# Optimization experiments

Hardware: AMD Instinct MI355X
Metric: run time of the kernel (lower is better)

Reference implementation:

```python
import jax, jax.numpy as jnp
import numpy as np

B, H, W, CIN, COUT, KH, KW = 8, 256, 256, 64, 64, 3, 3

def setup_inputs() -> dict:
    key = jax.random.key(0)
    k1, k2 = jax.random.split(key)
    inputs = jax.random.normal(k1, (B, H, W, CIN), dtype=jnp.float32)
    kernel = jax.random.normal(k2, (CIN, COUT, KH, KW), dtype=jnp.float32)
    return {"inputs": inputs, "kernel": kernel}

def reference(inputs, kernel):
    # Stride-1 transposed convolution with 'full' output size:
    # out[b, p, q, co] = sum_{ci,i,j} inputs[b, i, j, ci] * kernel[ci, co, p-i, q-j]
    # which is a full (mathematical) convolution. lax performs cross-correlation,
    # so flip the kernel spatially and pad by (k-1) on each side.
    kh, kw = kernel.shape[2], kernel.shape[3]
    k_flipped = jnp.flip(kernel, axis=(2, 3))
    out = jax.lax.conv_general_dilated(
        inputs, k_flipped,
        window_strides=(1, 1),
        padding=[(kh - 1, kh - 1), (kw - 1, kw - 1)],
        dimension_numbers=("NHWC", "IOHW", "NHWC"))
    # out: [B, H+KH-1, W+KW-1, COUT]; original call() adds no bias.
    return out
```

## Files before the change

kernel.cpp:

```cpp
#include <hip/hip_runtime.h>
#include <hip/hip_bf16.h>


#define OH 258
#define OW 258

typedef __bf16 bf16x8 __attribute__((ext_vector_type(8)));
typedef float  f32x4  __attribute__((ext_vector_type(4)));

__global__ void prep_w_kernel(const float* __restrict__ k, __bf16* __restrict__ wsW) {
    int i = blockIdx.x * 256 + threadIdx.x;
    int c  = i & 31;
    int co = (i >> 5) & 63;
    int st = i >> 11;
    int s   = st & 1;
    int tap = st >> 1;
    int kh = tap / 3, kw = tap % 3;
    float v = k[(s * 32 + c) * 576 + co * 9 + kh * 3 + kw];
    wsW[i] = (__bf16)v;
}

__global__ __launch_bounds__(1024, 4)
void tconv_kernel(const float* __restrict__ in, const __bf16* __restrict__ wsW,
                  float* __restrict__ out) {
    __shared__ __bf16 lds_in[612 * 64];
    __shared__ __bf16 lds_w[36864];

    const int tid = threadIdx.x;
    const int b  = blockIdx.z;
    const int p0 = blockIdx.y * 32;
    const int q0 = blockIdx.x * 16;

    #pragma unroll 1
    for (int k = 0; k < 5; ++k) {
        const int it = tid + k * 1024;
        const bool act = (k < 4) || (tid < 800);
        int pix = it >> 3, c8 = it & 7;
        int r = pix / 18, c = pix - r * 18;
        int ip = p0 - 2 + r, iq = q0 - 2 + c;
        f32x4 v0 = {0.f,0.f,0.f,0.f}, v1 = {0.f,0.f,0.f,0.f};
        if (act && (unsigned)ip < 256u && (unsigned)iq < 256u) {
            const float* g = in + (((size_t)b * 256 + ip) * 256 + iq) * 64 + c8 * 8;
            v0 = *(const f32x4*)g;
            v1 = *(const f32x4*)(g + 4);
        }
        if (act) {
            bf16x8 w;
            w[0]=(__bf16)v0[0]; w[1]=(__bf16)v0[1]; w[2]=(__bf16)v0[2]; w[3]=(__bf16)v0[3];
            w[4]=(__bf16)v1[0]; w[5]=(__bf16)v1[1]; w[6]=(__bf16)v1[2]; w[7]=(__bf16)v1[3];
            *(bf16x8*)&lds_in[pix * 64 + (c8 ^ (pix & 7)) * 8] = w;
        }
    }
    #pragma unroll
    for (int k = 0; k < 5; ++k) {
        const int g = tid + k * 1024;
        if ((k < 4) || (tid < 512))
            *(bf16x8*)&lds_w[(size_t)g * 8] = *(const bf16x8*)&wsW[(size_t)g * 8];
    }
    __syncthreads();

    const int wv = tid >> 6, lane = tid & 63;
    const int ml = lane & 15, h = lane >> 4;
    const int woff = ml * 32 + h * 8;
    const int rbase = wv * 2;

    f32x4 acc[2][4] = {};

    #pragma unroll 1
    for (int tap = 0; tap < 9; ++tap) {
        const int kh = tap / 3, kw = tap - kh * 3;
        const __bf16* wt = lds_w + tap * 4096;
        #pragma unroll
        for (int s = 0; s < 2; ++s) {
            bf16x8 bfr[4];
            #pragma unroll
            for (int nt = 0; nt < 4; ++nt)
                bfr[nt] = *(const bf16x8*)(wt + s * 2048 + nt * 512 + woff);
            const int j = s * 4 + h;
            #pragma unroll
            for (int mt = 0; mt < 2; ++mt) {
                int row = rbase + mt + 2 - kh;
                int pix = row * 18 + (2 - kw) + ml;
                bf16x8 afr = *(const bf16x8*)&lds_in[pix * 64 + ((j ^ (pix & 7)) * 8)];
                #pragma unroll
                for (int nt = 0; nt < 4; ++nt)
                    acc[mt][nt] = __builtin_amdgcn_mfma_f32_16x16x32_bf16(
                        bfr[nt], afr, acc[mt][nt], 0, 0, 0);
            }
        }
    }

    const int q = q0 + ml;
    #pragma unroll
    for (int mt = 0; mt < 2; ++mt) {
        int p = p0 + rbase + mt;
        if (p < OH && q < OW) {
            float* op = out + (((size_t)b * OH + p) * OW + q) * 64 + h * 4;
            #pragma unroll
            for (int nt = 0; nt < 4; ++nt)
                *(f32x4*)(op + nt * 16) = acc[mt][nt];
        }
    }
}

extern "C" void kernel_launch(void* const* d_in, const int* in_sizes, int n_in,
                              void* d_out, int out_size, void* d_ws, size_t ws_size,
                              hipStream_t stream) {
    (void)in_sizes; (void)n_in; (void)out_size; (void)ws_size;
    const float* in   = (const float*)d_in[0];
    const float* kern = (const float*)d_in[1];
    float* out = (float*)d_out;
    __bf16* wsW = (__bf16*)d_ws;

    prep_w_kernel<<<144, 256, 0, stream>>>(kern, wsW);
    dim3 grid(17, 9, 8);
    tconv_kernel<<<grid, 1024, 0, stream>>>(in, wsW, out);
}
```

Baseline: 257.3 us.

## Make conv kernel persistent with register-prefetched next-tile input patches

Replaces the 1224-block grid with 256 persistent blocks that each loop over 4-5 output tiles. Weights are loaded into LDS once per block, and the next tile's input patch is fetched into registers while the current tile's MFMAs run. The weight prep layout is also reordered so each lane's B-fragment reads are contiguous. The cost is higher register pressure from 40 prefetched float4 values per thread, an extra barrier per tile, and tail imbalance between 5-tile and 4-tile blocks.

```diff
diff --git a/kernel.cpp b/kernel.cpp
--- a/kernel.cpp
+++ b/kernel.cpp
@@ -10,14 +10,44 @@
 
 __global__ void prep_w_kernel(const float* __restrict__ k, __bf16* __restrict__ wsW) {
     int i = blockIdx.x * 256 + threadIdx.x;
-    int c  = i & 31;
-    int co = (i >> 5) & 63;
+    int j  = i & 7;
+    int ml = (i >> 3) & 15;
+    int h  = (i >> 7) & 3;
+    int nt = (i >> 9) & 3;
     int st = i >> 11;
-    int s   = st & 1;
-    int tap = st >> 1;
-    int kh = tap / 3, kw = tap % 3;
-    float v = k[(s * 32 + c) * 576 + co * 9 + kh * 3 + kw];
-    wsW[i] = (__bf16)v;
+    int s  = st & 1, tap = st >> 1;
+    int ci = s * 32 + h * 8 + j;
+    int co = nt * 16 + ml;
+    wsW[i] = (__bf16)k[ci * 576 + co * 9 + tap];
+}
+
+__device__ __forceinline__ void tile_coords(int tau, int& b, int& p0, int& q0) {
+    int bb = tau / 153;
+    int rr = tau - bb * 153;
+    int py = rr / 17;
+    b  = bb;
+    p0 = py * 32;
+    q0 = (rr - py * 17) * 16;
+}
+
+__device__ __forceinline__ void issue_patch_loads(
+        const float* __restrict__ in, int b, int p0, int q0, int tid,
+        f32x4 (&v0)[5], f32x4 (&v1)[5]) {
+    #pragma unroll
+    for (int k = 0; k < 5; ++k) {
+        const int it = tid + k * 1024;
+        const bool act = (k < 4) || (tid < 800);
+        int pix = it >> 3, c8 = it & 7;
+        int r = pix / 18, c = pix - r * 18;
+        int ip = p0 - 2 + r, iq = q0 - 2 + c;
+        f32x4 z = {0.f, 0.f, 0.f, 0.f};
+        v0[k] = z; v1[k] = z;
+        if (act && (unsigned)ip < 256u && (unsigned)iq < 256u) {
+            const float* g = in + (((size_t)b * 256 + ip) * 256 + iq) * 64 + c8 * 8;
+            v0[k] = *(const f32x4*)g;
+            v1[k] = *(const f32x4*)(g + 4);
+        }
+    }
 }
 
 __global__ __launch_bounds__(1024, 4)
@@ -27,79 +57,88 @@
     __shared__ __bf16 lds_w[36864];
 
     const int tid = threadIdx.x;
-    const int b  = blockIdx.z;
-    const int p0 = blockIdx.y * 32;
-    const int q0 = blockIdx.x * 16;
 
-    #pragma unroll 1
-    for (int k = 0; k < 5; ++k) {
-        const int it = tid + k * 1024;
-        const bool act = (k < 4) || (tid < 800);
-        int pix = it >> 3, c8 = it & 7;
-        int r = pix / 18, c = pix - r * 18;
-        int ip = p0 - 2 + r, iq = q0 - 2 + c;
-        f32x4 v0 = {0.f,0.f,0.f,0.f}, v1 = {0.f,0.f,0.f,0.f};
-        if (act && (unsigned)ip < 256u && (unsigned)iq < 256u) {
-            const float* g = in + (((size_t)b * 256 + ip) * 256 + iq) * 64 + c8 * 8;
-            v0 = *(const f32x4*)g;
-            v1 = *(const f32x4*)(g + 4);
-        }
-        if (act) {
-            bf16x8 w;
-            w[0]=(__bf16)v0[0]; w[1]=(__bf16)v0[1]; w[2]=(__bf16)v0[2]; w[3]=(__bf16)v0[3];
-            w[4]=(__bf16)v1[0]; w[5]=(__bf16)v1[1]; w[6]=(__bf16)v1[2]; w[7]=(__bf16)v1[3];
-            *(bf16x8*)&lds_in[pix * 64 + (c8 ^ (pix & 7)) * 8] = w;
-        }
-    }
     #pragma unroll
     for (int k = 0; k < 5; ++k) {
         const int g = tid + k * 1024;
         if ((k < 4) || (tid < 512))
             *(bf16x8*)&lds_w[(size_t)g * 8] = *(const bf16x8*)&wsW[(size_t)g * 8];
     }
-    __syncthreads();
 
     const int wv = tid >> 6, lane = tid & 63;
     const int ml = lane & 15, h = lane >> 4;
-    const int woff = ml * 32 + h * 8;
+    const int woff = h * 128 + ml * 8;
     const int rbase = wv * 2;
 
-    f32x4 acc[2][4] = {};
+    const int bx = blockIdx.x;
+    const int n_t = (bx < 200) ? 5 : 4;
+
+    int cb, cp0, cq0;
+    tile_coords(bx, cb, cp0, cq0);
+    f32x4 v0[5], v1[5];
+    issue_patch_loads(in, cb, cp0, cq0, tid, v0, v1);
+
+    int nb = 0, np0 = 0, nq0 = 0;
 
     #pragma unroll 1
-    for (int tap = 0; tap < 9; ++tap) {
-        const int kh = tap / 3, kw = tap - kh * 3;
-        const __bf16* wt = lds_w + tap * 4096;
+    for (int t = 0; t < n_t; ++t) {
+        __syncthreads();
         #pragma unroll
-        for (int s = 0; s < 2; ++s) {
-            bf16x8 bfr[4];
+        for (int k = 0; k < 5; ++k) {
+            const int it = tid + k * 1024;
+            if ((k < 4) || (tid < 800)) {
+                int pix = it >> 3, c8 = it & 7;
+                bf16x8 w;
+                w[0]=(__bf16)v0[k][0]; w[1]=(__bf16)v0[k][1];
+                w[2]=(__bf16)v0[k][2]; w[3]=(__bf16)v0[k][3];
+                w[4]=(__bf16)v1[k][0]; w[5]=(__bf16)v1[k][1];
+                w[6]=(__bf16)v1[k][2]; w[7]=(__bf16)v1[k][3];
+                *(bf16x8*)&lds_in[pix * 64 + ((c8 ^ (pix & 7)) * 8)] = w;
+            }
+        }
+        if (t + 1 < n_t) {
+            tile_coords(bx + (t + 1) * 256, nb, np0, nq0);
+            issue_patch_loads(in, nb, np0, nq0, tid, v0, v1);
+        }
+        __syncthreads();
+
+        f32x4 acc[2][4] = {};
+        #pragma unroll 1
+        for (int tap = 0; tap < 9; ++tap) {
+            const int kh = tap / 3, kw = tap - kh * 3;
+            const __bf16* wt = lds_w + tap * 4096;
             #pragma unroll
-            for (int nt = 0; nt < 4; ++nt)
-                bfr[nt] = *(const bf16x8*)(wt + s * 2048 + nt * 512 + woff);
-            const int j = s * 4 + h;
-            #pragma unroll
-            for (int mt = 0; mt < 2; ++mt) {
-                int row = rbase + mt + 2 - kh;
-                int pix = row * 18 + (2 - kw) + ml;
-                bf16x8 afr = *(const bf16x8*)&lds_in[pix * 64 + ((j ^ (pix & 7)) * 8)];
+            for (int s = 0; s < 2; ++s) {
+                bf16x8 bfr[4];
                 #pragma unroll
                 for (int nt = 0; nt < 4; ++nt)
-                    acc[mt][nt] = __builtin_amdgcn_mfma_f32_16x16x32_bf16(
-                        bfr[nt], afr, acc[mt][nt], 0, 0, 0);
+                    bfr[nt] = *(const bf16x8*)(wt + s * 2048 + nt * 512 + woff);
+                const int j = s * 4 + h;
+                #pragma unroll
+                for (int mt = 0; mt < 2; ++mt) {
+                    int row = rbase + mt + 2 - kh;
+                    int pix = row * 18 + (2 - kw) + ml;
+                    bf16x8 afr = *(const bf16x8*)&lds_in[pix * 64 + ((j ^ (pix & 7)) * 8)];
+                    #pragma unroll
+                    for (int nt = 0; nt < 4; ++nt)
+                        acc[mt][nt] = __builtin_amdgcn_mfma_f32_16x16x32_bf16(
+                            bfr[nt], afr, acc[mt][nt], 0, 0, 0);
+                }
             }
         }
-    }
 
-    const int q = q0 + ml;
-    #pragma unroll
-    for (int mt = 0; mt < 2; ++mt) {
-        int p = p0 + rbase + mt;
-        if (p < OH && q < OW) {
-            float* op = out + (((size_t)b * OH + p) * OW + q) * 64 + h * 4;
-            #pragma unroll
-            for (int nt = 0; nt < 4; ++nt)
-                *(f32x4*)(op + nt * 16) = acc[mt][nt];
+        const int q = cq0 + ml;
+        #pragma unroll
+        for (int mt = 0; mt < 2; ++mt) {
+            int p = cp0 + rbase + mt;
+            if (p < OH && q < OW) {
+                float* op = out + (((size_t)cb * OH + p) * OW + q) * 64 + h * 4;
+                #pragma unroll
+                for (int nt = 0; nt < 4; ++nt)
+                    *(f32x4*)(op + nt * 16) = acc[mt][nt];
+            }
         }
+        cb = nb; cp0 = np0; cq0 = nq0;
     }
 }
 
@@ -113,6 +152,5 @@
     __bf16* wsW = (__bf16*)d_ws;
 
     prep_w_kernel<<<144, 256, 0, stream>>>(kern, wsW);
-    dim3 grid(17, 9, 8);
-    tconv_kernel<<<grid, 1024, 0, stream>>>(in, wsW, out);
+    tconv_kernel<<<256, 1024, 0, stream>>>(in, wsW, out);
 }
```

Result: faster. 251.6 us (-2.2%).
